# Kernel optimization log

Measured on AMD Instinct MI355X. Metric: run time of the kernel, lower is better.

The kernel has to match this reference:

```python
import jax, jax.numpy as jnp
import numpy as np

C_IN, C_OUT, K, PAD, STRIDE = 128, 256, 3, 1, 1
H = W = 256


def setup_inputs() -> dict:
    key = jax.random.key(0)
    k1, k2, k3 = jax.random.split(key, 3)
    # batch=1: the original forward uses X_pad[0] for every batch index,
    # so with m=1 the buggy loop and a standard conv are mathematically identical.
    x = jax.random.normal(k1, (1, C_IN, H, W), dtype=jnp.float32)
    # nn.Parameter(torch.rand(...)) -> uniform[0,1)
    weight = jax.random.uniform(k2, (C_OUT, C_IN, K, K), dtype=jnp.float32)
    bias = jax.random.uniform(k3, (C_OUT,), dtype=jnp.float32)
    return {"x": x, "weight": weight, "bias": bias}


def reference(x, weight, bias):
    # Faithful math of convAppx.forward with FP_appx_mul treated as exact
    # multiply (FP_appx_mul is not defined in the source): a plain 2D
    # cross-correlation (no kernel flip, matching the sliced elementwise
    # product) with symmetric padding, stride 1, plus per-channel bias.
    z = jax.lax.conv_general_dilated(
        x, weight,
        window_strides=(STRIDE, STRIDE),
        padding=((PAD, PAD), (PAD, PAD)),
        dimension_numbers=("NCHW", "OIHW", "NCHW"),
    )
    return z + bias[None, :, None, None]
```

## Files before the change

### kernel.cpp

```cpp
#include <hip/hip_runtime.h>
#include <hip/hip_bf16.h>


typedef short bf16x8 __attribute__((ext_vector_type(8)));
typedef float f32x4 __attribute__((ext_vector_type(4)));
typedef unsigned short u16x4 __attribute__((ext_vector_type(4)));
typedef unsigned short u16x8 __attribute__((ext_vector_type(8)));

#define CIN   128
#define COUT  256
#define HH    256
#define WW    256
#define HP    258
#define ROWP  (HP * CIN)

static __device__ __forceinline__ unsigned short f2bf(float v) {
    __hip_bfloat16 b = __float2bfloat16(v);
    return *reinterpret_cast<unsigned short*>(&b);
}

__global__ __launch_bounds__(256) void xpose_kernel(const float* __restrict__ x,
                                                    unsigned short* __restrict__ xb) {
    int bid = blockIdx.x;
    int h  = bid >> 2;
    int w0 = (bid & 3) * 64;
    __shared__ unsigned short tile[CIN * 72];
    int t = threadIdx.x;

    int wq = t & 15;
    int cib = t >> 4;
    for (int c0 = 0; c0 < CIN; c0 += 16) {
        int ci = c0 + cib;
        float4 v = *(const float4*)(x + ci * (HH * WW) + h * WW + w0 + wq * 4);
        u16x4 p;
        p.x = f2bf(v.x); p.y = f2bf(v.y); p.z = f2bf(v.z); p.w = f2bf(v.w);
        *(u16x4*)(&tile[ci * 72 + wq * 4]) = p;
    }
    __syncthreads();

    for (int it = 0; it < 4; ++it) {
        int idx = it * 256 + t;
        int w  = idx >> 4;
        int c8 = idx & 15;
        u16x8 o;
        #pragma unroll
        for (int j = 0; j < 8; ++j)
            o[j] = tile[(c8 * 8 + j) * 72 + w];
        int dst = ((h + 1) * HP + (w0 + w + 1)) * CIN + c8 * 8;
        *(u16x8*)(&xb[dst]) = o;
    }
}

__global__ __launch_bounds__(256) void zero_edges_kernel(unsigned short* __restrict__ xb) {
    int i = blockIdx.x * 256 + threadIdx.x;
    if (i >= 16448) return;
    u16x8 z = {0, 0, 0, 0, 0, 0, 0, 0};
    int off;
    if (i < 8256) {
        int r   = (i >= 4128) ? 1 : 0;
        int rem = i - r * 4128;
        off = (r * 257) * ROWP + rem * 8;
    } else {
        int j   = i - 8256;
        int col = j >> 12;
        int rem = j & 4095;
        int hp  = (rem >> 4) + 1;
        int c8  = rem & 15;
        off = hp * ROWP + (col * 257) * CIN + c8 * 8;
    }
    *(u16x8*)(&xb[off]) = z;
}

__global__ __launch_bounds__(256) void wreorder_kernel(const float* __restrict__ w,
                                                       unsigned short* __restrict__ wr) {
    int i = blockIdx.x * 256 + threadIdx.x;
    int khw = i >> 15;
    int rem = i & 32767;
    int co  = rem >> 7;
    int ci  = rem & 127;
    wr[i] = f2bf(w[co * (CIN * 9) + ci * 9 + khw]);
}

#define LROW 72

__global__ __launch_bounds__(256) void conv_mfma_kernel(const unsigned short* __restrict__ xb,
                                                        const unsigned short* __restrict__ wr,
                                                        const float* __restrict__ bias,
                                                        float* __restrict__ out) {
    __shared__ unsigned short As[128 * LROW];
    __shared__ unsigned short Bs[128 * LROW];

    int bid  = blockIdx.x;
    int co_t = bid & 1;
    int wh   = (bid >> 1) & 1;
    int h    = bid >> 2;
    int co0  = co_t * 128;
    int p0   = h * WW + wh * 128;

    int t    = threadIdx.x;
    int wave = t >> 6;
    int lane = t & 63;
    int wm   = wave >> 1;
    int wn   = wave & 1;
    int quad = lane >> 4;
    int l16  = lane & 15;

    f32x4 acc[4][4];
    #pragma unroll
    for (int mi = 0; mi < 4; ++mi)
        #pragma unroll
        for (int ni = 0; ni < 4; ++ni)
            acc[mi][ni] = (f32x4){0.f, 0.f, 0.f, 0.f};

    for (int kh = 0; kh < 3; ++kh) {
        for (int kw = 0; kw < 3; ++kw) {
            int khw = kh * 3 + kw;
            const unsigned short* xsrc = xb + ((h + kh) * HP + wh * 128 + kw) * CIN;
            const unsigned short* wsrc = wr + khw * (COUT * CIN) + co0 * CIN;
            for (int cc = 0; cc < 2; ++cc) {
                int kofs = cc * 64;
                __syncthreads();
                #pragma unroll
                for (int it = 0; it < 4; ++it) {
                    int seg = it * 256 + t;
                    int r = seg >> 3;
                    int s = seg & 7;
                    int ge = kofs + s * 8;
                    float4 av = *(const float4*)(wsrc + r * CIN + ge);
                    float4 bv = *(const float4*)(xsrc + r * CIN + ge);
                    *(float4*)(&As[r * LROW + s * 8]) = av;
                    *(float4*)(&Bs[r * LROW + s * 8]) = bv;
                }
                __syncthreads();
                #pragma unroll
                for (int kk = 0; kk < 2; ++kk) {
                    bf16x8 af[4], bfr[4];
                    #pragma unroll
                    for (int mi = 0; mi < 4; ++mi)
                        af[mi] = *(bf16x8*)(&As[(wm * 64 + mi * 16 + l16) * LROW + kk * 32 + quad * 8]);
                    #pragma unroll
                    for (int ni = 0; ni < 4; ++ni)
                        bfr[ni] = *(bf16x8*)(&Bs[(wn * 64 + ni * 16 + l16) * LROW + kk * 32 + quad * 8]);
                    #pragma unroll
                    for (int mi = 0; mi < 4; ++mi)
                        #pragma unroll
                        for (int ni = 0; ni < 4; ++ni)
                            acc[mi][ni] = __builtin_amdgcn_mfma_f32_16x16x32_bf16(
                                af[mi], bfr[ni], acc[mi][ni], 0, 0, 0);
                }
            }
        }
    }

    #pragma unroll
    for (int mi = 0; mi < 4; ++mi) {
        #pragma unroll
        for (int r = 0; r < 4; ++r) {
            int co = co0 + wm * 64 + mi * 16 + quad * 4 + r;
            float b = bias[co];
            float* orow = out + co * (HH * WW) + p0 + wn * 64 + l16;
            #pragma unroll
            for (int ni = 0; ni < 4; ++ni)
                orow[ni * 16] = acc[mi][ni][r] + b;
        }
    }
}

extern "C" void kernel_launch(void* const* d_in, const int* in_sizes, int n_in,
                              void* d_out, int out_size, void* d_ws, size_t ws_size,
                              hipStream_t stream) {
    const float* x    = (const float*)d_in[0];
    const float* w    = (const float*)d_in[1];
    const float* bias = (const float*)d_in[2];
    float* out        = (float*)d_out;

    unsigned short* xb = (unsigned short*)d_ws;
    unsigned short* wr = xb + (size_t)HP * HP * CIN;

    xpose_kernel<<<dim3(1024), dim3(256), 0, stream>>>(x, xb);
    zero_edges_kernel<<<dim3(65), dim3(256), 0, stream>>>(xb);
    wreorder_kernel<<<dim3(1152), dim3(256), 0, stream>>>(w, wr);
    conv_mfma_kernel<<<dim3(1024), dim3(256), 0, stream>>>(xb, wr, bias, out);
}
```

Baseline: 146.7 us.

## Use direct global-to-LDS loads with XOR-swizzled tiles, retune transpose and weight reorder

The conv kernel now stages A and B tiles with global_load_lds 16-byte transfers straight into LDS instead of going through registers. Tiles are unpadded with an XOR swizzle to avoid bank conflicts on the MFMA fragment reads. The transpose kernel's write mapping is changed so consecutive threads write consecutive pixels, and the weight reorder reads each contiguous 9-element filter once per thread. The swizzle and the per-wave LDS layout must exactly match the layout global_load_lds writes, so any mismatch would corrupt the staged tiles.

```diff
diff --git a/kernel.cpp b/kernel.cpp
--- a/kernel.cpp
+++ b/kernel.cpp
@@ -17,6 +17,12 @@
 static __device__ __forceinline__ unsigned short f2bf(float v) {
     __hip_bfloat16 b = __float2bfloat16(v);
     return *reinterpret_cast<unsigned short*>(&b);
+}
+
+static __device__ __forceinline__ void gload_lds16(const unsigned short* g, unsigned short* l) {
+    __builtin_amdgcn_global_load_lds(
+        (const __attribute__((address_space(1))) unsigned int*)g,
+        (__attribute__((address_space(3))) unsigned int*)l, 16, 0, 0);
 }
 
 __global__ __launch_bounds__(256) void xpose_kernel(const float* __restrict__ x,
@@ -40,8 +46,8 @@
 
     for (int it = 0; it < 4; ++it) {
         int idx = it * 256 + t;
-        int w  = idx >> 4;
-        int c8 = idx & 15;
+        int w  = idx & 63;
+        int c8 = idx >> 6;
         u16x8 o;
         #pragma unroll
         for (int j = 0; j < 8; ++j)
@@ -73,22 +79,19 @@
 
 __global__ __launch_bounds__(256) void wreorder_kernel(const float* __restrict__ w,
                                                        unsigned short* __restrict__ wr) {
-    int i = blockIdx.x * 256 + threadIdx.x;
-    int khw = i >> 15;
-    int rem = i & 32767;
-    int co  = rem >> 7;
-    int ci  = rem & 127;
-    wr[i] = f2bf(w[co * (CIN * 9) + ci * 9 + khw]);
+    int p = blockIdx.x * 256 + threadIdx.x;
+    const float* src = w + p * 9;
+    #pragma unroll
+    for (int khw = 0; khw < 9; ++khw)
+        wr[khw * (COUT * CIN) + p] = f2bf(src[khw]);
 }
-
-#define LROW 72
 
 __global__ __launch_bounds__(256) void conv_mfma_kernel(const unsigned short* __restrict__ xb,
                                                         const unsigned short* __restrict__ wr,
                                                         const float* __restrict__ bias,
                                                         float* __restrict__ out) {
-    __shared__ unsigned short As[128 * LROW];
-    __shared__ unsigned short Bs[128 * LROW];
+    __shared__ unsigned short As[128 * 64];
+    __shared__ unsigned short Bs[128 * 64];
 
     int bid  = blockIdx.x;
     int co_t = bid & 1;
@@ -104,6 +107,11 @@
     int wn   = wave & 1;
     int quad = lane >> 4;
     int l16  = lane & 15;
+    int sw   = l16 & 7;
+
+    int lr = lane >> 3;
+    int s  = lane & 7;
+    int cs = (s ^ lr) * 8;
 
     f32x4 acc[4][4];
     #pragma unroll
@@ -122,25 +130,26 @@
                 __syncthreads();
                 #pragma unroll
                 for (int it = 0; it < 4; ++it) {
-                    int seg = it * 256 + t;
-                    int r = seg >> 3;
-                    int s = seg & 7;
-                    int ge = kofs + s * 8;
-                    float4 av = *(const float4*)(wsrc + r * CIN + ge);
-                    float4 bv = *(const float4*)(xsrc + r * CIN + ge);
-                    *(float4*)(&As[r * LROW + s * 8]) = av;
-                    *(float4*)(&Bs[r * LROW + s * 8]) = bv;
+                    int cid = wave * 4 + it;
+                    int r   = cid * 8 + lr;
+                    int ge  = kofs + cs;
+                    gload_lds16(wsrc + r * CIN + ge, &As[cid * 512]);
+                    gload_lds16(xsrc + r * CIN + ge, &Bs[cid * 512]);
                 }
                 __syncthreads();
                 #pragma unroll
                 for (int kk = 0; kk < 2; ++kk) {
                     bf16x8 af[4], bfr[4];
                     #pragma unroll
-                    for (int mi = 0; mi < 4; ++mi)
-                        af[mi] = *(bf16x8*)(&As[(wm * 64 + mi * 16 + l16) * LROW + kk * 32 + quad * 8]);
+                    for (int mi = 0; mi < 4; ++mi) {
+                        int row = wm * 64 + mi * 16 + l16;
+                        af[mi] = *(bf16x8*)(&As[row * 64 + ((kk * 4 + quad) ^ sw) * 8]);
+                    }
                     #pragma unroll
-                    for (int ni = 0; ni < 4; ++ni)
-                        bfr[ni] = *(bf16x8*)(&Bs[(wn * 64 + ni * 16 + l16) * LROW + kk * 32 + quad * 8]);
+                    for (int ni = 0; ni < 4; ++ni) {
+                        int row = wn * 64 + ni * 16 + l16;
+                        bfr[ni] = *(bf16x8*)(&Bs[row * 64 + ((kk * 4 + quad) ^ sw) * 8]);
+                    }
                     #pragma unroll
                     for (int mi = 0; mi < 4; ++mi)
                         #pragma unroll
@@ -179,6 +188,6 @@
 
     xpose_kernel<<<dim3(1024), dim3(256), 0, stream>>>(x, xb);
     zero_edges_kernel<<<dim3(65), dim3(256), 0, stream>>>(xb);
-    wreorder_kernel<<<dim3(1152), dim3(256), 0, stream>>>(w, wr);
+    wreorder_kernel<<<dim3(128), dim3(256), 0, stream>>>(w, wr);
     conv_mfma_kernel<<<dim3(1024), dim3(256), 0, stream>>>(xb, wr, bias, out);
 }
```

Measured after the change: 143.4 us. -2.2%, faster.
